# Kernel optimization log

Measured on AMD Instinct MI355X. Metric: run time of the kernel, lower is better.

The kernel has to match this reference:

```python
import jax, jax.numpy as jnp
import numpy as np


def setup_inputs() -> dict:
    key = jax.random.key(0)
    k1, k2, k3 = jax.random.split(key, 3)
    dim, heads, dim_head, rows = 512, 8, 64, 64
    b, t = 4, 256
    _dim = heads * dim_head
    x = jax.random.normal(k1, (b * rows, t, dim), dtype=jnp.float32)
    # torch nn.Linear weight layout: [out_features, in_features]
    W_qkv = jax.random.normal(k2, (3 * _dim, dim), dtype=jnp.float32) * (dim ** -0.5)
    W0 = jax.random.normal(k3, (dim, _dim), dtype=jnp.float32) * (_dim ** -0.5)
    return {"x": x, "W_qkv": W_qkv, "W0": W0, "rows": rows, "heads": heads}


def reference(x, W_qkv, W0, rows, heads):
    br, t, dim = x.shape
    b = br // rows
    three_dim = W_qkv.shape[0]
    dim_head = three_dim // (3 * heads)
    scale = (rows * dim_head) ** -0.5

    qkv = x @ W_qkv.T  # [(b*rows), t, 3*heads*dim_head]
    # einops '(b rows) t (d k h) -> k b rows h t d': last dim ordered (d, k, h)
    qkv = qkv.reshape(b, rows, t, dim_head, 3, heads)
    qkv = jnp.transpose(qkv, (4, 0, 1, 5, 2, 3))  # [3, b, rows, h, t, d]
    q, k, v = qkv[0], qkv[1], qkv[2]

    # tied-row attention: sum QK^T over rows before a single shared softmax
    scores = jnp.einsum('brhid,brhjd->bhij', q, k) * scale  # [b, h, t, t]
    attn = jax.nn.softmax(scores, axis=-1)
    # broadcast shared attention map back across rows
    out = jnp.einsum('bhij,brhjd->brhid', attn, v)  # [b, rows, h, t, d]
    # 'b rows h t d -> (b rows) t (h d)'
    out = jnp.transpose(out, (0, 1, 3, 2, 4)).reshape(br, t, heads * dim_head)
    return out @ W0.T
```

## Files before the change

### kernel.cpp

```cpp
#include <hip/hip_runtime.h>


typedef short  bf16x8 __attribute__((ext_vector_type(8)));
typedef float  f32x4  __attribute__((ext_vector_type(4)));

#define MFMA16(a,b,c) __builtin_amdgcn_mfma_f32_16x16x32_bf16((a),(b),(c),0,0,0)

__device__ __forceinline__ ushort f2bf(float f) {
  union { float f; unsigned u; } v; v.f = f;
  unsigned r = v.u + 0x7fffu + ((v.u >> 16) & 1u);
  return (ushort)(r >> 16);
}

__device__ __forceinline__ void gload_lds16(const void* g, void* lds) {
  __builtin_amdgcn_global_load_lds(
      (const __attribute__((address_space(1))) void*)g,
      (__attribute__((address_space(3))) void*)lds, 16, 0, 0);
}


__global__ void cast_f32_to_bf16(const float* __restrict__ in,
                                 ushort* __restrict__ out, int n4) {
  int idx = blockIdx.x * blockDim.x + threadIdx.x;
  int stride = gridDim.x * blockDim.x;
  for (int v = idx; v < n4; v += stride) {
    float4 f = reinterpret_cast<const float4*>(in)[v];
    ushort4 o; o.x = f2bf(f.x); o.y = f2bf(f.y); o.z = f2bf(f.z); o.w = f2bf(f.w);
    reinterpret_cast<ushort4*>(out)[v] = o;
  }
}

__global__ void permute_wqkv_k(const float* __restrict__ W, ushort* __restrict__ Wp) {
  int np = blockIdx.x;
  int k = np >> 9, h = (np >> 6) & 7, d = np & 63;
  const float4* s = reinterpret_cast<const float4*>(W + (size_t)(d * 24 + k * 8 + h) * 512);
  ushort4* o = reinterpret_cast<ushort4*>(Wp + (size_t)np * 512);
  for (int c = threadIdx.x; c < 128; c += blockDim.x) {
    float4 f = s[c];
    ushort4 u; u.x = f2bf(f.x); u.y = f2bf(f.y); u.z = f2bf(f.z); u.w = f2bf(f.w);
    o[c] = u;
  }
}


__device__ __forceinline__ void gemm_nt_512x128(
    const ushort* __restrict__ A, const ushort* __restrict__ B,
    int lda, int ldb, int P, int m0, int n0, char* lds, f32x4 (&acc)[8][4]) {
  const int tid = threadIdx.x;
  const int w = tid >> 6, l = tid & 63;
  const int il = l & 15, kl = l >> 4;
  const int wm = w >> 1, wn = w & 1;

  auto stageA_half = [&](char* buf, int kt, int half) {
#pragma unroll
    for (int c = 0; c < 2; ++c) {
      int rbase = (half << 8) + (w << 5) + (c << 4);
      int row = rbase + (l >> 2);
      int s = ((l & 3) - ((row >> 1) & 3)) & 3;
      const ushort* g = A + (size_t)(m0 + row) * lda + (kt << 5) + (s << 3);
      gload_lds16(g, buf + rbase * 64);
    }
  };
  auto stageB = [&](char* buf, int kt) {
    int rbase = (w << 4);
    int row = rbase + (l >> 2);
    int s = ((l & 3) - ((row >> 1) & 3)) & 3;
    const ushort* g = B + (size_t)(n0 + row) * ldb + (kt << 5) + (s << 3);
    gload_lds16(g, buf + 32768 + rbase * 64);
  };
  auto loadA4 = [&](const char* abuf, int fmbase, bf16x8 (&af)[4]) {
#pragma unroll
    for (int q = 0; q < 4; ++q) {
      int row = (wm << 7) + ((fmbase + q) << 4) + il;
      af[q] = *(const bf16x8*)(abuf + row * 64 + (((kl + (row >> 1)) & 3) << 4));
    }
  };
  auto loadB4 = [&](const char* bbuf, bf16x8 (&bfr)[4]) {
#pragma unroll
    for (int q = 0; q < 4; ++q) {
      int row = (wn << 6) + (q << 4) + il;
      bfr[q] = *(const bf16x8*)(bbuf + 32768 + row * 64 + (((kl + (row >> 1)) & 3) << 4));
    }
  };

#pragma unroll
  for (int i = 0; i < 8; ++i)
#pragma unroll
    for (int j = 0; j < 4; ++j) acc[i][j] = f32x4{0.f, 0.f, 0.f, 0.f};

  {
    char* b0 = lds;
    char* b1 = lds + 40960;
    stageA_half(b0, 0, 0); stageB(b0, 0); stageA_half(b0, 0, 1);
    stageA_half(b1, 1, 0); stageB(b1, 1); stageA_half(b1, 1, 1);
    asm volatile("s_waitcnt vmcnt(5)" ::: "memory");
    __builtin_amdgcn_s_barrier();
  }

  int cur = 0, n2 = 2;
  for (int g = 0; g < P; ++g) {
    char* cbuf = lds + cur * 40960;
    char* sbuf = lds + n2 * 40960;
    const bool pf = (g + 2 < P);
    bf16x8 bfr[4];
    {
      bf16x8 af[4];
      loadA4(cbuf, 0, af);
      loadB4(cbuf, bfr);
      if (pf) { stageA_half(sbuf, g + 2, 0); stageB(sbuf, g + 2); }
      __builtin_amdgcn_s_barrier();
      asm volatile("s_waitcnt lgkmcnt(0)" ::: "memory");
      __builtin_amdgcn_sched_barrier(0);
      __builtin_amdgcn_s_setprio(1);
#pragma unroll
      for (int fm = 0; fm < 4; ++fm)
#pragma unroll
        for (int fn = 0; fn < 4; ++fn)
          acc[fm][fn] = MFMA16(af[fm], bfr[fn], acc[fm][fn]);
      __builtin_amdgcn_s_setprio(0);
      __builtin_amdgcn_s_barrier();
    }
    {
      bf16x8 af[4];
      loadA4(cbuf, 4, af);
      if (pf) stageA_half(sbuf, g + 2, 1);
      if (pf)                asm volatile("s_waitcnt vmcnt(5)" ::: "memory");
      else if (g + 1 < P)    asm volatile("s_waitcnt vmcnt(0)" ::: "memory");
      __builtin_amdgcn_s_barrier();
      asm volatile("s_waitcnt lgkmcnt(0)" ::: "memory");
      __builtin_amdgcn_sched_barrier(0);
      __builtin_amdgcn_s_setprio(1);
#pragma unroll
      for (int fm = 0; fm < 4; ++fm)
#pragma unroll
        for (int fn = 0; fn < 4; ++fn)
          acc[4 + fm][fn] = MFMA16(af[fm], bfr[fn], acc[4 + fm][fn]);
      __builtin_amdgcn_s_setprio(0);
      __builtin_amdgcn_s_barrier();
    }
    cur = (cur == 2) ? 0 : cur + 1;
    n2  = (n2  == 2) ? 0 : n2  + 1;
  }
}


__global__ __launch_bounds__(512, 2) void gemm_qkv_k(
    const ushort* __restrict__ xb, const ushort* __restrict__ Wp,
    ushort* __restrict__ Qb, ushort* __restrict__ Kb, ushort* __restrict__ Vt) {
  __shared__ __align__(16) char lds[122880];
  f32x4 acc[8][4];
  const int Bid = blockIdx.x;
  const int xcd = Bid & 7, idx = Bid >> 3;
  const int nt = idx % 12, pl = idx / 12;
  const int m0 = ((pl << 3) + xcd) << 9;
  const int n0 = nt << 7;
  gemm_nt_512x128(xb, Wp, 512, 512, 16, m0, n0, lds, acc);

  const int tid = threadIdx.x, w = tid >> 6, l = tid & 63;
  const int il = l & 15, kl = l >> 4;
  const int wm = w >> 1, wn = w & 1;
  const int kq = n0 >> 9;

  if (kq < 2) {
    ushort* dstb = kq ? Kb : Qb;
#pragma unroll
    for (int fm = 0; fm < 8; ++fm)
#pragma unroll
      for (int fn = 0; fn < 4; ++fn) {
        int n = n0 + (wn << 6) + (fn << 4) + il;
        int h = (n >> 6) & 7, d = n & 63;
#pragma unroll
        for (int j = 0; j < 4; ++j) {
          int m = m0 + (wm << 7) + (fm << 4) + (kl << 2) + j;
          int i = m & 255, br = m >> 8, b = br >> 6, r = br & 63;
          size_t dst = ((size_t)((((b << 3) + h) << 8) + i) << 12) + (r << 6) + d;
          dstb[dst] = f2bf(acc[fm][fn][j]);
        }
      }
  } else {
#pragma unroll
    for (int fm = 0; fm < 8; ++fm)
#pragma unroll
      for (int fn = 0; fn < 4; ++fn) {
        int n = n0 - 1024 + (wn << 6) + (fn << 4) + il;
        int h = n >> 6, d = n & 63;
        int m = m0 + (wm << 7) + (fm << 4) + (kl << 2);
        int i0 = m & 255, br = m >> 8, b = br >> 6, r = br & 63;
        size_t dst = (((size_t)((((b << 3) + h) << 12)) + (r << 6) + d) << 8) + i0;
        ushort4 pk; pk.x = f2bf(acc[fm][fn][0]); pk.y = f2bf(acc[fm][fn][1]);
        pk.z = f2bf(acc[fm][fn][2]); pk.w = f2bf(acc[fm][fn][3]);
        *reinterpret_cast<ushort4*>(&Vt[dst]) = pk;
      }
  }
}


__global__ __launch_bounds__(512, 2) void gemm_out_k(
    const ushort* __restrict__ O2, const ushort* __restrict__ W0b,
    float* __restrict__ out) {
  __shared__ __align__(16) char lds[122880];
  f32x4 acc[8][4];
  const int Bid = blockIdx.x;
  const int xcd = Bid & 7, idx = Bid >> 3;
  const int nt = idx & 3, pl = idx >> 2;
  const int m0 = ((pl << 3) + xcd) << 9;
  const int n0 = nt << 7;
  gemm_nt_512x128(O2, W0b, 512, 512, 16, m0, n0, lds, acc);

  const int tid = threadIdx.x, w = tid >> 6, l = tid & 63;
  const int il = l & 15, kl = l >> 4;
  const int wm = w >> 1, wn = w & 1;
#pragma unroll
  for (int fm = 0; fm < 8; ++fm)
#pragma unroll
    for (int fn = 0; fn < 4; ++fn) {
      int n = n0 + (wn << 6) + (fn << 4) + il;
#pragma unroll
      for (int j = 0; j < 4; ++j) {
        int m = m0 + (wm << 7) + (fm << 4) + (kl << 2) + j;
        out[(size_t)m * 512 + n] = acc[fm][fn][j];
      }
    }
}


__device__ __forceinline__ void gemm_nt_mainloop_128(
    const ushort* __restrict__ A, const ushort* __restrict__ B,
    int lda, int ldb, int klen, int m0, int n0, ushort* lds, f32x4 (&acc)[4][4]) {
  const int tid = threadIdx.x;
  const int w = tid >> 6, l = tid & 63;
  const int il = l & 15, kl = l >> 4;

  ushort* ldsA[2] = { lds,         lds + 8192  };
  ushort* ldsB[2] = { lds + 16384, lds + 24576 };

  int srow[4], scs[4], sbase[4];
#pragma unroll
  for (int q = 0; q < 4; ++q) {
    int wb = ((q * 4 + w) << 10);
    int o  = wb + (l << 4);
    int row = o >> 7, c = o & 127;
    srow[q] = row; scs[q] = c ^ ((row & 7) << 4); sbase[q] = wb;
  }

#pragma unroll
  for (int i = 0; i < 4; ++i)
#pragma unroll
    for (int j = 0; j < 4; ++j) acc[i][j] = f32x4{0.f, 0.f, 0.f, 0.f};

  const int NT = klen >> 6;
  const int wr = (w >> 1) << 6, wc = (w & 1) << 6;

  auto stage = [&](int buf, int kt) {
    int kb = kt << 6;
#pragma unroll
    for (int q = 0; q < 4; ++q) {
      gload_lds16(A + (size_t)(m0 + srow[q]) * lda + kb + (scs[q] >> 1),
                  (char*)ldsA[buf] + sbase[q]);
      gload_lds16(B + (size_t)(n0 + srow[q]) * ldb + kb + (scs[q] >> 1),
                  (char*)ldsB[buf] + sbase[q]);
    }
  };

  stage(0, 0);
  __syncthreads();
  for (int kt = 0; kt < NT; ++kt) {
    if (kt + 1 < NT) stage((kt + 1) & 1, kt + 1);
    const ushort* la = ldsA[kt & 1];
    const ushort* lb = ldsB[kt & 1];
    bf16x8 af[2][4], bfr[2][4];
#pragma unroll
    for (int fm = 0; fm < 4; ++fm) {
      int row = wr + (fm << 4) + il, sw = (row & 7) << 4;
#pragma unroll
      for (int kk = 0; kk < 2; ++kk)
        af[kk][fm] = *(const bf16x8*)((const char*)la + row * 128 + ((((kk << 6) + (kl << 4))) ^ sw));
    }
#pragma unroll
    for (int fn = 0; fn < 4; ++fn) {
      int row = wc + (fn << 4) + il, sw = (row & 7) << 4;
#pragma unroll
      for (int kk = 0; kk < 2; ++kk)
        bfr[kk][fn] = *(const bf16x8*)((const char*)lb + row * 128 + ((((kk << 6) + (kl << 4))) ^ sw));
    }
#pragma unroll
    for (int kk = 0; kk < 2; ++kk)
#pragma unroll
      for (int fm = 0; fm < 4; ++fm)
#pragma unroll
        for (int fn = 0; fn < 4; ++fn)
          acc[fm][fn] = MFMA16(af[kk][fm], bfr[kk][fn], acc[fm][fn]);
    __syncthreads();
  }
}


__global__ __launch_bounds__(256, 2) void gemm_s_k(
    const ushort* __restrict__ Qb, const ushort* __restrict__ Kb,
    float* __restrict__ Sp) {
  __shared__ __align__(16) ushort lds[32768];
  f32x4 acc[4][4];
  const int Bid = blockIdx.x;
  const int xcd = Bid & 7, idx = Bid >> 3;
  const int sub = idx & 3, zl = idx >> 2;
  const int z = (zl << 3) + xcd;
  const int bh = z >> 2, ks = z & 3;
  const int m0 = (sub & 1) << 7, n0 = (sub >> 1) << 7;
  const size_t base = ((size_t)bh << 20) + ((size_t)ks << 10);
  gemm_nt_mainloop_128(Qb + base, Kb + base, 4096, 4096, 1024, m0, n0, lds, acc);

  const int tid = threadIdx.x, w = tid >> 6, l = tid & 63;
  const int il = l & 15, kl = l >> 4;
  const int wr = (w >> 1) << 6, wc = (w & 1) << 6;
  float* out = Sp + ((size_t)z << 16);
#pragma unroll
  for (int fm = 0; fm < 4; ++fm)
#pragma unroll
    for (int fn = 0; fn < 4; ++fn) {
      int n = n0 + wc + (fn << 4) + il;
#pragma unroll
      for (int j = 0; j < 4; ++j) {
        int m = m0 + wr + (fm << 4) + (kl << 2) + j;
        out[(size_t)m * 256 + n] = acc[fm][fn][j];
      }
    }
}


__global__ void softmax_k(const float* __restrict__ Sp, ushort* __restrict__ Pb) {
  const int w = threadIdx.x >> 6, l = threadIdx.x & 63;
  const int row = (blockIdx.x << 2) + w;
  const int bh = row >> 8, i = row & 255;
  const float4* p0 = reinterpret_cast<const float4*>(
      Sp + (((size_t)bh << 2) << 16) + ((size_t)i << 8)) + l;
  float4 a = p0[0], b2 = p0[16384], c = p0[32768], d = p0[49152];
  const float scale = 0.015625f;
  float s0 = (a.x + b2.x + c.x + d.x) * scale;
  float s1 = (a.y + b2.y + c.y + d.y) * scale;
  float s2 = (a.z + b2.z + c.z + d.z) * scale;
  float s3 = (a.w + b2.w + c.w + d.w) * scale;
  float m = fmaxf(fmaxf(s0, s1), fmaxf(s2, s3));
#pragma unroll
  for (int d2 = 1; d2 < 64; d2 <<= 1) m = fmaxf(m, __shfl_xor(m, d2));
  float e0 = __expf(s0 - m), e1 = __expf(s1 - m);
  float e2 = __expf(s2 - m), e3 = __expf(s3 - m);
  float sum = e0 + e1 + e2 + e3;
#pragma unroll
  for (int d2 = 1; d2 < 64; d2 <<= 1) sum += __shfl_xor(sum, d2);
  float r = 1.0f / sum;
  ushort4 p; p.x = f2bf(e0 * r); p.y = f2bf(e1 * r);
  p.z = f2bf(e2 * r); p.w = f2bf(e3 * r);
  reinterpret_cast<ushort4*>(Pb + ((size_t)bh << 16) + ((size_t)i << 8))[l] = p;
}


__global__ __launch_bounds__(256, 2) void gemm_pv_k(
    const ushort* __restrict__ Vt, const ushort* __restrict__ Pb,
    ushort* __restrict__ O2) {
  __shared__ __align__(16) ushort lds[32768];
  f32x4 acc[4][4];
  const int bh = blockIdx.z, b = bh >> 3, h = bh & 7;
  const int m0 = blockIdx.x << 7;
  const int n0 = blockIdx.y << 7;
  gemm_nt_mainloop_128(Vt + ((size_t)bh << 20), Pb + ((size_t)bh << 16),
                       256, 256, 256, m0, n0, lds, acc);

  const int tid = threadIdx.x, w = tid >> 6, l = tid & 63;
  const int il = l & 15, kl = l >> 4;
  const int wr = (w >> 1) << 6, wc = (w & 1) << 6;
#pragma unroll
  for (int fm = 0; fm < 4; ++fm) {
    int rd0 = m0 + wr + (fm << 4) + (kl << 2);
    int r = rd0 >> 6, d0 = rd0 & 63;
#pragma unroll
    for (int fn = 0; fn < 4; ++fn) {
      int i = n0 + wc + (fn << 4) + il;
      ushort4 pk; pk.x = f2bf(acc[fm][fn][0]); pk.y = f2bf(acc[fm][fn][1]);
      pk.z = f2bf(acc[fm][fn][2]); pk.w = f2bf(acc[fm][fn][3]);
      *reinterpret_cast<ushort4*>(
          O2 + ((size_t)((((b << 6) + r) << 8) + i) << 9) + (h << 6) + d0) = pk;
    }
  }
}


extern "C" void kernel_launch(void* const* d_in, const int* in_sizes, int n_in,
                              void* d_out, int out_size, void* d_ws, size_t ws_size,
                              hipStream_t stream) {
  const float* x    = (const float*)d_in[0];
  const float* Wqkv = (const float*)d_in[1];
  const float* W0   = (const float*)d_in[2];
  float* out = (float*)d_out;

  char* ws = (char*)d_ws;
  ushort* xb  = (ushort*)(ws);
  ushort* Wp  = (ushort*)(ws + 67108864);
  ushort* W0b = (ushort*)(ws + 68681728);
  ushort* Qb  = (ushort*)(ws + 69206016);
  ushort* Kb  = (ushort*)(ws + 136314880);
  ushort* Vt  = (ushort*)(ws + 203423744);
  if (ws_size < 270532608ull) return;

  cast_f32_to_bf16<<<2048, 256, 0, stream>>>(x, xb, 8388608);
  cast_f32_to_bf16<<<256, 256, 0, stream>>>(W0, W0b, 65536);
  permute_wqkv_k<<<1536, 128, 0, stream>>>(Wqkv, Wp);

  gemm_qkv_k<<<1536, 512, 0, stream>>>(xb, Wp, Qb, Kb, Vt);

  float*  Sp = (float*)xb;
  ushort* Pb = Qb;
  ushort* O2 = xb;

  gemm_s_k<<<512, 256, 0, stream>>>(Qb, Kb, Sp);
  softmax_k<<<2048, 256, 0, stream>>>(Sp, Pb);
  gemm_pv_k<<<dim3(32, 2, 32), 256, 0, stream>>>(Vt, Pb, O2);

  gemm_out_k<<<512, 512, 0, stream>>>(O2, W0b, out);
}
```

Baseline: 313.4 us.

## Swap MFMA operands for vectorized epilogue stores and retile PV GEMM

Adds a swap flag that exchanges the MFMA A/B operands, so each lane's four accumulators run along the output's contiguous dimension. This lets the Q/K, S and output epilogues write packed ushort4/float4 stores instead of scattered scalar ones. The PV GEMM moves from the 128x128 double-buffered mainloop onto the 512x128 triple-buffered pipelined kernel with XCD-aware block mapping. Risks include lower occupancy and fewer blocks for PV, and index remapping errors in the transposed epilogues.

Measured after the change: 370.7 us. 1.18x slower.

```diff
diff --git a/kernel.cpp b/kernel.cpp
--- a/kernel.cpp
+++ b/kernel.cpp
@@ -45,7 +45,8 @@
 
 __device__ __forceinline__ void gemm_nt_512x128(
     const ushort* __restrict__ A, const ushort* __restrict__ B,
-    int lda, int ldb, int P, int m0, int n0, char* lds, f32x4 (&acc)[8][4]) {
+    int lda, int ldb, int P, int m0, int n0, char* lds, bool swap,
+    f32x4 (&acc)[8][4]) {
   const int tid = threadIdx.x;
   const int w = tid >> 6, l = tid & 63;
   const int il = l & 15, kl = l >> 4;
@@ -112,11 +113,19 @@
       asm volatile("s_waitcnt lgkmcnt(0)" ::: "memory");
       __builtin_amdgcn_sched_barrier(0);
       __builtin_amdgcn_s_setprio(1);
-#pragma unroll
-      for (int fm = 0; fm < 4; ++fm)
-#pragma unroll
-        for (int fn = 0; fn < 4; ++fn)
-          acc[fm][fn] = MFMA16(af[fm], bfr[fn], acc[fm][fn]);
+      if (swap) {
+#pragma unroll
+        for (int fm = 0; fm < 4; ++fm)
+#pragma unroll
+          for (int fn = 0; fn < 4; ++fn)
+            acc[fm][fn] = MFMA16(bfr[fn], af[fm], acc[fm][fn]);
+      } else {
+#pragma unroll
+        for (int fm = 0; fm < 4; ++fm)
+#pragma unroll
+          for (int fn = 0; fn < 4; ++fn)
+            acc[fm][fn] = MFMA16(af[fm], bfr[fn], acc[fm][fn]);
+      }
       __builtin_amdgcn_s_setprio(0);
       __builtin_amdgcn_s_barrier();
     }
@@ -130,11 +139,19 @@
       asm volatile("s_waitcnt lgkmcnt(0)" ::: "memory");
       __builtin_amdgcn_sched_barrier(0);
       __builtin_amdgcn_s_setprio(1);
-#pragma unroll
-      for (int fm = 0; fm < 4; ++fm)
-#pragma unroll
-        for (int fn = 0; fn < 4; ++fn)
-          acc[4 + fm][fn] = MFMA16(af[fm], bfr[fn], acc[4 + fm][fn]);
+      if (swap) {
+#pragma unroll
+        for (int fm = 0; fm < 4; ++fm)
+#pragma unroll
+          for (int fn = 0; fn < 4; ++fn)
+            acc[4 + fm][fn] = MFMA16(bfr[fn], af[fm], acc[4 + fm][fn]);
+      } else {
+#pragma unroll
+        for (int fm = 0; fm < 4; ++fm)
+#pragma unroll
+          for (int fn = 0; fn < 4; ++fn)
+            acc[4 + fm][fn] = MFMA16(af[fm], bfr[fn], acc[4 + fm][fn]);
+      }
       __builtin_amdgcn_s_setprio(0);
       __builtin_amdgcn_s_barrier();
     }
@@ -154,29 +171,30 @@
   const int nt = idx % 12, pl = idx / 12;
   const int m0 = ((pl << 3) + xcd) << 9;
   const int n0 = nt << 7;
-  gemm_nt_512x128(xb, Wp, 512, 512, 16, m0, n0, lds, acc);
+  const int kq = n0 >> 9;
+  gemm_nt_512x128(xb, Wp, 512, 512, 16, m0, n0, lds, kq < 2, acc);
 
   const int tid = threadIdx.x, w = tid >> 6, l = tid & 63;
   const int il = l & 15, kl = l >> 4;
   const int wm = w >> 1, wn = w & 1;
-  const int kq = n0 >> 9;
 
   if (kq < 2) {
     ushort* dstb = kq ? Kb : Qb;
 #pragma unroll
-    for (int fm = 0; fm < 8; ++fm)
+    for (int fm = 0; fm < 8; ++fm) {
+      int m = m0 + (wm << 7) + (fm << 4) + il;
+      int i = m & 255, br = m >> 8, b = br >> 6, r = br & 63;
+      int h_i_base = (((b << 3)) << 8) + i;
 #pragma unroll
       for (int fn = 0; fn < 4; ++fn) {
-        int n = n0 + (wn << 6) + (fn << 4) + il;
-        int h = (n >> 6) & 7, d = n & 63;
-#pragma unroll
-        for (int j = 0; j < 4; ++j) {
-          int m = m0 + (wm << 7) + (fm << 4) + (kl << 2) + j;
-          int i = m & 255, br = m >> 8, b = br >> 6, r = br & 63;
-          size_t dst = ((size_t)((((b << 3) + h) << 8) + i) << 12) + (r << 6) + d;
-          dstb[dst] = f2bf(acc[fm][fn][j]);
-        }
+        int n = n0 + (wn << 6) + (fn << 4) + (kl << 2);
+        int h = (n >> 6) & 7, d0 = n & 63;
+        size_t dst = ((size_t)(h_i_base + (h << 8)) << 12) + (r << 6) + d0;
+        ushort4 pk; pk.x = f2bf(acc[fm][fn][0]); pk.y = f2bf(acc[fm][fn][1]);
+        pk.z = f2bf(acc[fm][fn][2]); pk.w = f2bf(acc[fm][fn][3]);
+        *reinterpret_cast<ushort4*>(&dstb[dst]) = pk;
       }
+    }
   } else {
 #pragma unroll
     for (int fm = 0; fm < 8; ++fm)
@@ -205,28 +223,60 @@
   const int nt = idx & 3, pl = idx >> 2;
   const int m0 = ((pl << 3) + xcd) << 9;
   const int n0 = nt << 7;
-  gemm_nt_512x128(O2, W0b, 512, 512, 16, m0, n0, lds, acc);
+  gemm_nt_512x128(O2, W0b, 512, 512, 16, m0, n0, lds, true, acc);
 
   const int tid = threadIdx.x, w = tid >> 6, l = tid & 63;
   const int il = l & 15, kl = l >> 4;
   const int wm = w >> 1, wn = w & 1;
 #pragma unroll
-  for (int fm = 0; fm < 8; ++fm)
+  for (int fm = 0; fm < 8; ++fm) {
+    int m = m0 + (wm << 7) + (fm << 4) + il;
 #pragma unroll
     for (int fn = 0; fn < 4; ++fn) {
-      int n = n0 + (wn << 6) + (fn << 4) + il;
-#pragma unroll
-      for (int j = 0; j < 4; ++j) {
-        int m = m0 + (wm << 7) + (fm << 4) + (kl << 2) + j;
-        out[(size_t)m * 512 + n] = acc[fm][fn][j];
-      }
-    }
+      int n = n0 + (wn << 6) + (fn << 4) + (kl << 2);
+      *reinterpret_cast<f32x4*>(&out[(size_t)m * 512 + n]) = acc[fm][fn];
+    }
+  }
+}
+
+
+__global__ __launch_bounds__(512, 2) void gemm_pv_k(
+    const ushort* __restrict__ Vt, const ushort* __restrict__ Pb,
+    ushort* __restrict__ O2) {
+  __shared__ __align__(16) char lds[122880];
+  f32x4 acc[8][4];
+  const int Bid = blockIdx.x;
+  const int xcd = Bid & 7, idx = Bid >> 3;
+  const int sub = idx & 15, grp = idx >> 4;
+  const int bh = (grp << 3) + xcd, b = bh >> 3, h = bh & 7;
+  const int m0 = (sub >> 1) << 9;
+  const int n0 = (sub & 1) << 7;
+  gemm_nt_512x128(Vt + ((size_t)bh << 20), Pb + ((size_t)bh << 16),
+                  256, 256, 8, m0, n0, lds, false, acc);
+
+  const int tid = threadIdx.x, w = tid >> 6, l = tid & 63;
+  const int il = l & 15, kl = l >> 4;
+  const int wm = w >> 1, wn = w & 1;
+#pragma unroll
+  for (int fm = 0; fm < 8; ++fm) {
+    int rd0 = m0 + (wm << 7) + (fm << 4) + (kl << 2);
+    int r = rd0 >> 6, d0 = rd0 & 63;
+#pragma unroll
+    for (int fn = 0; fn < 4; ++fn) {
+      int i = n0 + (wn << 6) + (fn << 4) + il;
+      ushort4 pk; pk.x = f2bf(acc[fm][fn][0]); pk.y = f2bf(acc[fm][fn][1]);
+      pk.z = f2bf(acc[fm][fn][2]); pk.w = f2bf(acc[fm][fn][3]);
+      *reinterpret_cast<ushort4*>(
+          O2 + ((size_t)((((b << 6) + r) << 8) + i) << 9) + (h << 6) + d0) = pk;
+    }
+  }
 }
 
 
 __device__ __forceinline__ void gemm_nt_mainloop_128(
     const ushort* __restrict__ A, const ushort* __restrict__ B,
-    int lda, int ldb, int klen, int m0, int n0, ushort* lds, f32x4 (&acc)[4][4]) {
+    int lda, int ldb, int klen, int m0, int n0, ushort* lds, bool swap,
+    f32x4 (&acc)[4][4]) {
   const int tid = threadIdx.x;
   const int w = tid >> 6, l = tid & 63;
   const int il = l & 15, kl = l >> 4;
@@ -283,13 +333,23 @@
       for (int kk = 0; kk < 2; ++kk)
         bfr[kk][fn] = *(const bf16x8*)((const char*)lb + row * 128 + ((((kk << 6) + (kl << 4))) ^ sw));
     }
-#pragma unroll
-    for (int kk = 0; kk < 2; ++kk)
-#pragma unroll
-      for (int fm = 0; fm < 4; ++fm)
-#pragma unroll
-        for (int fn = 0; fn < 4; ++fn)
-          acc[fm][fn] = MFMA16(af[kk][fm], bfr[kk][fn], acc[fm][fn]);
+    if (swap) {
+#pragma unroll
+      for (int kk = 0; kk < 2; ++kk)
+#pragma unroll
+        for (int fm = 0; fm < 4; ++fm)
+#pragma unroll
+          for (int fn = 0; fn < 4; ++fn)
+            acc[fm][fn] = MFMA16(bfr[kk][fn], af[kk][fm], acc[fm][fn]);
+    } else {
+#pragma unroll
+      for (int kk = 0; kk < 2; ++kk)
+#pragma unroll
+        for (int fm = 0; fm < 4; ++fm)
+#pragma unroll
+          for (int fn = 0; fn < 4; ++fn)
+            acc[fm][fn] = MFMA16(af[kk][fm], bfr[kk][fn], acc[fm][fn]);
+    }
     __syncthreads();
   }
 }
@@ -307,23 +367,22 @@
   const int bh = z >> 2, ks = z & 3;
   const int m0 = (sub & 1) << 7, n0 = (sub >> 1) << 7;
   const size_t base = ((size_t)bh << 20) + ((size_t)ks << 10);
-  gemm_nt_mainloop_128(Qb + base, Kb + base, 4096, 4096, 1024, m0, n0, lds, acc);
+  gemm_nt_mainloop_128(Qb + base, Kb + base, 4096, 4096, 1024, m0, n0, lds,
+                       true, acc);
 
   const int tid = threadIdx.x, w = tid >> 6, l = tid & 63;
   const int il = l & 15, kl = l >> 4;
   const int wr = (w >> 1) << 6, wc = (w & 1) << 6;
   float* out = Sp + ((size_t)z << 16);
 #pragma unroll
-  for (int fm = 0; fm < 4; ++fm)
+  for (int fm = 0; fm < 4; ++fm) {
+    int m = m0 + wr + (fm << 4) + il;
 #pragma unroll
     for (int fn = 0; fn < 4; ++fn) {
-      int n = n0 + wc + (fn << 4) + il;
-#pragma unroll
-      for (int j = 0; j < 4; ++j) {
-        int m = m0 + wr + (fm << 4) + (kl << 2) + j;
-        out[(size_t)m * 256 + n] = acc[fm][fn][j];
-      }
-    }
+      int n = n0 + wc + (fn << 4) + (kl << 2);
+      *reinterpret_cast<f32x4*>(&out[(size_t)m * 256 + n]) = acc[fm][fn];
+    }
+  }
 }
 
 
@@ -354,36 +413,6 @@
 }
 
 
-__global__ __launch_bounds__(256, 2) void gemm_pv_k(
-    const ushort* __restrict__ Vt, const ushort* __restrict__ Pb,
-    ushort* __restrict__ O2) {
-  __shared__ __align__(16) ushort lds[32768];
-  f32x4 acc[4][4];
-  const int bh = blockIdx.z, b = bh >> 3, h = bh & 7;
-  const int m0 = blockIdx.x << 7;
-  const int n0 = blockIdx.y << 7;
-  gemm_nt_mainloop_128(Vt + ((size_t)bh << 20), Pb + ((size_t)bh << 16),
-                       256, 256, 256, m0, n0, lds, acc);
-
-  const int tid = threadIdx.x, w = tid >> 6, l = tid & 63;
-  const int il = l & 15, kl = l >> 4;
-  const int wr = (w >> 1) << 6, wc = (w & 1) << 6;
-#pragma unroll
-  for (int fm = 0; fm < 4; ++fm) {
-    int rd0 = m0 + wr + (fm << 4) + (kl << 2);
-    int r = rd0 >> 6, d0 = rd0 & 63;
-#pragma unroll
-    for (int fn = 0; fn < 4; ++fn) {
-      int i = n0 + wc + (fn << 4) + il;
-      ushort4 pk; pk.x = f2bf(acc[fm][fn][0]); pk.y = f2bf(acc[fm][fn][1]);
-      pk.z = f2bf(acc[fm][fn][2]); pk.w = f2bf(acc[fm][fn][3]);
-      *reinterpret_cast<ushort4*>(
-          O2 + ((size_t)((((b << 6) + r) << 8) + i) << 9) + (h << 6) + d0) = pk;
-    }
-  }
-}
-
-
 extern "C" void kernel_launch(void* const* d_in, const int* in_sizes, int n_in,
                               void* d_out, int out_size, void* d_ws, size_t ws_size,
                               hipStream_t stream) {
@@ -413,7 +442,7 @@
 
   gemm_s_k<<<512, 256, 0, stream>>>(Qb, Kb, Sp);
   softmax_k<<<2048, 256, 0, stream>>>(Sp, Pb);
-  gemm_pv_k<<<dim3(32, 2, 32), 256, 0, stream>>>(Vt, Pb, O2);
+  gemm_pv_k<<<512, 512, 0, stream>>>(Vt, Pb, O2);
 
   gemm_out_k<<<512, 512, 0, stream>>>(O2, W0b, out);
 }
```
